# Performance work log

Measured on AMD Instinct MI355X. Metric: run time of the kernel, lower is better.

Reference implementation:

```python
import jax, jax.numpy as jnp
import numpy as np

B, S, D, KC = 32, 4096, 64, 256  # batch*heads, seq_len, head_dim, compressed dim


def setup_inputs() -> dict:
    key = jax.random.key(0)
    ks = jax.random.split(key, 7)
    return {
        "Q": jax.random.normal(ks[0], (B, S, D), dtype=jnp.float32),
        "K": jax.random.normal(ks[1], (B, S, D), dtype=jnp.float32),
        "V": jax.random.normal(ks[2], (B, S, D), dtype=jnp.float32),
        "E_w": jax.random.normal(ks[3], (KC, S), dtype=jnp.float32) * (1.0 / np.sqrt(S)),
        "E_b": jax.random.normal(ks[4], (KC,), dtype=jnp.float32) * 0.01,
        "F_w": jax.random.normal(ks[5], (KC, S), dtype=jnp.float32) * (1.0 / np.sqrt(S)),
        "F_b": jax.random.normal(ks[6], (KC,), dtype=jnp.float32) * 0.01,
    }


def reference(Q, K, V, E_w, E_b, F_w, F_b):
    # K: [B,S,D] -> transpose -> [B,D,S]; E proj over seq axis -> [B,D,KC]
    Ke = jnp.einsum("bsd,ks->bdk", K, E_w) + E_b  # [B, D, KC]
    # scores: Q @ E(K) -> [B, S, KC], scaled by sqrt(head_dim)
    scale = jnp.sqrt(jnp.asarray(D, dtype=Q.dtype))
    P = jnp.einsum("bsd,bdk->bsk", Q, Ke) / scale
    # causal mask: torch.triu(ones(S, KC)) keeps (i, j) where j >= i
    i = jnp.arange(S)[:, None]
    j = jnp.arange(KC)[None, :]
    keep = j >= i  # [S, KC]
    P = jnp.where(keep[None, :, :], P, jnp.asarray(-1e10, dtype=P.dtype))
    P = jax.nn.softmax(P, axis=-1)  # dropout p=0.0 -> identity
    # V: [B,S,D] -> [B,D,S]; F proj -> [B,D,KC]; transpose -> [B,KC,D]
    Vf = jnp.einsum("bsd,ks->bkd", V, F_w) + F_b[None, :, None]  # [B, KC, D]
    out = jnp.einsum("bsk,bkd->bsd", P, Vf)  # [B, S, D]
    return out
```

## Files before the change

kernel.cpp:

```cpp
#include <hip/hip_runtime.h>
#include <hip/hip_bf16.h>
#include <math.h>

#define NB  32
#define NS  4096
#define ND  64
#define NKC 256

#define BK    128
#define KHALF 2048
#define ASA   132
#define ASB   132

#define QSTR  72
#define PBSTR 264
#define VSTR  264

#define NKE ((size_t)NB * NKC * ND)

typedef __attribute__((ext_vector_type(8))) short short8;
typedef __attribute__((ext_vector_type(4))) float f32x4;

__device__ __forceinline__ short f2bf(float f) {
    union { float f; unsigned u; } v; v.f = f;
    return (short)((v.u + 0x7FFFu + ((v.u >> 16) & 1u)) >> 16);
}

template <typename AT>
__global__ __launch_bounds__(256, 2) void proj_sk(
    const AT* __restrict__ EwX, const AT* __restrict__ FwX,
    const float* __restrict__ K, const float* __restrict__ V,
    float* __restrict__ base)
{
    const int bid = blockIdx.x;
    const int r8 = bid & 7, mt = (bid >> 3) & 3, gq = bid >> 5;
    const int grp = gq * 8 + r8;
    const int kh = grp & 1, mm = (grp >> 1) & 1, b = grp >> 2;

    const AT* __restrict__ Ab    = mm ? FwX : EwX;
    const float* __restrict__ Bg = mm ? V   : K;
    float* __restrict__ Cout = base + (size_t)kh * 2 * NKE + (mm ? NKE : 0);

    const int t = threadIdx.x, wave = t >> 6, lane = t & 63;
    const int lm = lane & 15, g4 = lane >> 4;
    __shared__ short As[64 * ASA];
    __shared__ short Bs[64 * ASB];
    const size_t bBase = (size_t)b * NS * ND;
    const size_t aBase = (size_t)mt * 64 * NS;
    const int rA = t >> 4, jA = t & 15;
    const int dB = t & 31, sB = t >> 5;

    f32x4 acc[4];
#pragma unroll
    for (int nt = 0; nt < 4; ++nt) acc[nt] = (f32x4){0.f, 0.f, 0.f, 0.f};

    short8 pa[4];
    float4 paf[8];
    float2 pb[16];

    const int sBeg = kh * KHALF, sEnd = sBeg + KHALF;

#pragma unroll
    for (int i = 0; i < 4; ++i) {
        if constexpr (sizeof(AT) == 2) {
            pa[i] = *(const short8*)&Ab[aBase + (size_t)(i * 16 + rA) * NS + sBeg + jA * 8];
        } else {
            paf[2 * i]     = *(const float4*)&Ab[aBase + (size_t)(i * 16 + rA) * NS + sBeg + jA * 8];
            paf[2 * i + 1] = *(const float4*)&Ab[aBase + (size_t)(i * 16 + rA) * NS + sBeg + jA * 8 + 4];
        }
    }
#pragma unroll
    for (int h = 0; h < 2; ++h)
#pragma unroll
        for (int i = 0; i < 8; ++i)
            pb[h * 8 + i] = *(const float2*)&Bg[bBase + (size_t)(sBeg + h * 64 + sB * 8 + i) * ND + dB * 2];

    for (int s0 = sBeg; s0 < sEnd; s0 += BK) {
#pragma unroll
        for (int i = 0; i < 4; ++i) {
            if constexpr (sizeof(AT) == 2) {
                *(short8*)&As[(i * 16 + rA) * ASA + jA * 8] = pa[i];
            } else {
                short8 w;
                w[0] = f2bf(paf[2 * i].x);     w[1] = f2bf(paf[2 * i].y);
                w[2] = f2bf(paf[2 * i].z);     w[3] = f2bf(paf[2 * i].w);
                w[4] = f2bf(paf[2 * i + 1].x); w[5] = f2bf(paf[2 * i + 1].y);
                w[6] = f2bf(paf[2 * i + 1].z); w[7] = f2bf(paf[2 * i + 1].w);
                *(short8*)&As[(i * 16 + rA) * ASA + jA * 8] = w;
            }
        }
#pragma unroll
        for (int h = 0; h < 2; ++h) {
            short8 w0, w1;
#pragma unroll
            for (int i = 0; i < 8; ++i) {
                w0[i] = f2bf(pb[h * 8 + i].x);
                w1[i] = f2bf(pb[h * 8 + i].y);
            }
            *(short8*)&Bs[(dB * 2 + 0) * ASB + h * 64 + sB * 8] = w0;
            *(short8*)&Bs[(dB * 2 + 1) * ASB + h * 64 + sB * 8] = w1;
        }
        __syncthreads();

        if (s0 + BK < sEnd) {
            const int sn = s0 + BK;
#pragma unroll
            for (int i = 0; i < 4; ++i) {
                if constexpr (sizeof(AT) == 2) {
                    pa[i] = *(const short8*)&Ab[aBase + (size_t)(i * 16 + rA) * NS + sn + jA * 8];
                } else {
                    paf[2 * i]     = *(const float4*)&Ab[aBase + (size_t)(i * 16 + rA) * NS + sn + jA * 8];
                    paf[2 * i + 1] = *(const float4*)&Ab[aBase + (size_t)(i * 16 + rA) * NS + sn + jA * 8 + 4];
                }
            }
#pragma unroll
            for (int h = 0; h < 2; ++h)
#pragma unroll
                for (int i = 0; i < 8; ++i)
                    pb[h * 8 + i] = *(const float2*)&Bg[bBase + (size_t)(sn + h * 64 + sB * 8 + i) * ND + dB * 2];
        }

#pragma unroll
        for (int ks = 0; ks < BK; ks += 32) {
            short8 aF = *(const short8*)&As[(wave * 16 + lm) * ASA + ks + g4 * 8];
#pragma unroll
            for (int nt = 0; nt < 4; ++nt) {
                short8 bF = *(const short8*)&Bs[(nt * 16 + lm) * ASB + ks + g4 * 8];
                acc[nt] = __builtin_amdgcn_mfma_f32_16x16x32_bf16(aF, bF, acc[nt], 0, 0, 0);
            }
        }
        __syncthreads();
    }

#pragma unroll
    for (int nt = 0; nt < 4; ++nt)
#pragma unroll
        for (int rr = 0; rr < 4; ++rr) {
            int kc = mt * 64 + wave * 16 + g4 * 4 + rr;
            Cout[((size_t)b * NKC + kc) * ND + nt * 16 + lm] = acc[nt][rr];
        }
}

__global__ __launch_bounds__(256) void fuse(
    const float* __restrict__ base, const float* __restrict__ Eb,
    const float* __restrict__ Fb, short* __restrict__ KeB,
    short* __restrict__ VtB, float* __restrict__ ps)
{
    const int x = blockIdx.x, b = blockIdx.y, t = threadIdx.x;
    const int kb = x * 16;
    const float* Ka  = base;
    const float* Va  = base + NKE;
    const float* Kb_ = base + 2 * NKE;
    const float* Vb  = base + 3 * NKE;
    __shared__ float vt[16][65];
    const int kci = t >> 6, d = t & 63;

#pragma unroll
    for (int i = 0; i < 4; ++i) {
        int kc = kb + kci * 4 + i;
        size_t off = ((size_t)b * NKC + kc) * ND + d;
        KeB[off] = f2bf(Ka[off] + Kb_[off] + Eb[kc]);
        vt[kci * 4 + i][d] = Va[off] + Vb[off] + Fb[kc];
    }
    __syncthreads();
    if (t < 64) {
        float s = 0.f;
        short8 w0, w1;
#pragma unroll
        for (int i = 0; i < 8; ++i) { float v = vt[i][t];     s += v; w0[i] = f2bf(v); }
#pragma unroll
        for (int i = 0; i < 8; ++i) { float v = vt[8 + i][t]; s += v; w1[i] = f2bf(v); }
        ps[((size_t)b * 16 + x) * 64 + t] = s;
        short* dst = &VtB[((size_t)b * ND + t) * NKC + kb];
        *(short8*)&dst[0] = w0;
        *(short8*)&dst[8] = w1;
    }
}

__global__ __launch_bounds__(256) void attn_new(
    const float* __restrict__ Q,  const short* __restrict__ KeB,
    const short* __restrict__ VtB, const float* __restrict__ ps,
    float* __restrict__ out)
{
    const int x = blockIdx.x, b = blockIdx.y, t = threadIdx.x;

    if (x >= 8) {
        __shared__ float mvs[64];
        if (t < 64) {
            float s = 0.f;
#pragma unroll
            for (int i = 0; i < 16; ++i) s += ps[((size_t)b * 16 + i) * 64 + t];
            mvs[t] = s * (1.f / 256.f);
        }
        __syncthreads();
        const int r0 = 256 + (x - 8) * 64;
#pragma unroll
        for (int i = 0; i < 4; ++i) {
            int idx = i * 256 + t, row = idx >> 4, q = idx & 15;
            *(float4*)&out[((size_t)b * NS + r0 + row) * ND + q * 4] =
                *(const float4*)&mvs[q * 4];
        }
        return;
    }

    const int s0 = x * 32;
    const int wave = t >> 6, lane = t & 63, lm = lane & 15, g = lane >> 4;
    __shared__ short Qs[32 * QSTR];
    __shared__ short PsB[32 * PBSTR];
    __shared__ short VfT[64 * VSTR];
    __shared__ float rsums[32][4];

    {
        int row = t >> 3, dq = t & 7;
        size_t off = ((size_t)b * NS + s0 + row) * ND + dq * 8;
        float4 q0 = *(const float4*)&Q[off], q1 = *(const float4*)&Q[off + 4];
        short8 w;
        w[0] = f2bf(q0.x); w[1] = f2bf(q0.y); w[2] = f2bf(q0.z); w[3] = f2bf(q0.w);
        w[4] = f2bf(q1.x); w[5] = f2bf(q1.y); w[6] = f2bf(q1.z); w[7] = f2bf(q1.w);
        *(short8*)&Qs[row * QSTR + dq * 8] = w;
    }
    {
        const int d = t >> 2, q4 = t & 3;
        const short* src = &VtB[((size_t)b * ND + d) * NKC + q4 * 64];
#pragma unroll
        for (int i = 0; i < 8; ++i)
            *(short8*)&VfT[d * VSTR + q4 * 64 + i * 8] = *(const short8*)&src[i * 8];
    }
    __syncthreads();

    f32x4 accP[2][4];
#pragma unroll
    for (int rt = 0; rt < 2; ++rt)
#pragma unroll
        for (int kk = 0; kk < 4; ++kk) accP[rt][kk] = (f32x4){0.f, 0.f, 0.f, 0.f};
#pragma unroll
    for (int kk = 0; kk < 4; ++kk) {
        int kt = wave * 4 + kk;
#pragma unroll
        for (int ks2 = 0; ks2 < 2; ++ks2) {
            short8 bf = *(const short8*)&KeB[((size_t)b * NKC + kt * 16 + lm) * ND + ks2 * 32 + g * 8];
#pragma unroll
            for (int rt = 0; rt < 2; ++rt) {
                short8 aq = *(const short8*)&Qs[(rt * 16 + lm) * QSTR + ks2 * 32 + g * 8];
                accP[rt][kk] = __builtin_amdgcn_mfma_f32_16x16x32_bf16(aq, bf, accP[rt][kk], 0, 0, 0);
            }
        }
    }
#pragma unroll
    for (int rt = 0; rt < 2; ++rt)
#pragma unroll
        for (int r = 0; r < 4; ++r) {
            float s = 0.f;
            int rowg = s0 + rt * 16 + g * 4 + r;
#pragma unroll
            for (int kk = 0; kk < 4; ++kk) {
                int col = wave * 64 + kk * 16 + lm;
                float e = (col >= rowg) ? __expf(accP[rt][kk][r] * 0.125f) : 0.f;
                accP[rt][kk][r] = e;
                s += e;
            }
#pragma unroll
            for (int off = 1; off <= 8; off <<= 1) s += __shfl_xor(s, off, 64);
            if (lm == 0) rsums[rt * 16 + g * 4 + r][wave] = s;
        }
    __syncthreads();
#pragma unroll
    for (int rt = 0; rt < 2; ++rt)
#pragma unroll
        for (int r = 0; r < 4; ++r) {
            float4 rs = *(const float4*)&rsums[rt * 16 + g * 4 + r][0];
            float inv = 1.f / (rs.x + rs.y + rs.z + rs.w);
#pragma unroll
            for (int kk = 0; kk < 4; ++kk)
                PsB[(rt * 16 + g * 4 + r) * PBSTR + wave * 64 + kk * 16 + lm] =
                    f2bf(accP[rt][kk][r] * inv);
        }
    __syncthreads();

    f32x4 oa[2];
    oa[0] = (f32x4){0.f, 0.f, 0.f, 0.f};
    oa[1] = (f32x4){0.f, 0.f, 0.f, 0.f};
    for (int ks = x; ks < 8; ++ks) {
        short8 bv = *(const short8*)&VfT[(wave * 16 + lm) * VSTR + ks * 32 + g * 8];
#pragma unroll
        for (int rt = 0; rt < 2; ++rt) {
            short8 av = *(const short8*)&PsB[(rt * 16 + lm) * PBSTR + ks * 32 + g * 8];
            oa[rt] = __builtin_amdgcn_mfma_f32_16x16x32_bf16(av, bv, oa[rt], 0, 0, 0);
        }
    }
#pragma unroll
    for (int rt = 0; rt < 2; ++rt)
#pragma unroll
        for (int r = 0; r < 4; ++r)
            out[((size_t)b * NS + s0 + rt * 16 + g * 4 + r) * ND + wave * 16 + lm] = oa[rt][r];
}

__global__ __launch_bounds__(256) void attn_old(
    const float* __restrict__ Q,  const float* __restrict__ base,
    const float* __restrict__ Eb, const float* __restrict__ Fb,
    float* __restrict__ out)
{
    const int x = blockIdx.x, b = blockIdx.y, t = threadIdx.x;
    const float* KeTa = base;
    const float* Vfa  = base + NKE;
    const float* KeTb = base + 2 * NKE;
    const float* Vfb  = base + 3 * NKE;

    if (x >= 8) {
        __shared__ float pq[16][64];
        __shared__ float mvs[64];
        const int kg = t >> 4, dq = t & 15;
        float4 s4 = (float4){0.f, 0.f, 0.f, 0.f};
        for (int p = 0; p < 16; ++p) {
            int k = p * 16 + kg;
            float4 v = *(const float4*)&Vfa[((size_t)b * NKC + k) * ND + dq * 4];
            float4 u = *(const float4*)&Vfb[((size_t)b * NKC + k) * ND + dq * 4];
            float fb = Fb[k];
            s4.x += (v.x + u.x) + fb; s4.y += (v.y + u.y) + fb;
            s4.z += (v.z + u.z) + fb; s4.w += (v.w + u.w) + fb;
        }
        *(float4*)&pq[kg][dq * 4] = s4;
        __syncthreads();
        if (t < 64) {
            float m = 0.f;
#pragma unroll
            for (int i = 0; i < 16; ++i) m += pq[i][t];
            mvs[t] = m * (1.f / 256.f);
        }
        __syncthreads();
        const int r0 = 256 + (x - 8) * 64;
#pragma unroll
        for (int i = 0; i < 4; ++i) {
            int idx = i * 256 + t, row = idx >> 4, q = idx & 15;
            *(float4*)&out[((size_t)b * NS + r0 + row) * ND + q * 4] =
                *(const float4*)&mvs[q * 4];
        }
        return;
    }

    const int s0 = x * 32;
    const int wave = t >> 6, lane = t & 63, lm = lane & 15, g = lane >> 4;
    __shared__ short Qs[32 * QSTR];
    __shared__ short PsB[32 * PBSTR];
    __shared__ short VfT[64 * VSTR];
    __shared__ float rsums[32][4];

    {
        int row = t >> 3, dq = t & 7;
        size_t off = ((size_t)b * NS + s0 + row) * ND + dq * 8;
        float4 q0 = *(const float4*)&Q[off], q1 = *(const float4*)&Q[off + 4];
        short8 w;
        w[0] = f2bf(q0.x); w[1] = f2bf(q0.y); w[2] = f2bf(q0.z); w[3] = f2bf(q0.w);
        w[4] = f2bf(q1.x); w[5] = f2bf(q1.y); w[6] = f2bf(q1.z); w[7] = f2bf(q1.w);
        *(short8*)&Qs[row * QSTR + dq * 8] = w;
    }
    {
        const int dB = t & 31, sB = t >> 5;
#pragma unroll
        for (int pass = 0; pass < 4; ++pass) {
            int kb = pass * 64 + sB * 8;
            float2 v[8]; float fb[8];
#pragma unroll
            for (int i = 0; i < 8; ++i) {
                float2 a = *(const float2*)&Vfa[((size_t)b * NKC + kb + i) * ND + dB * 2];
                float2 c = *(const float2*)&Vfb[((size_t)b * NKC + kb + i) * ND + dB * 2];
                v[i]  = (float2){a.x + c.x, a.y + c.y};
                fb[i] = Fb[kb + i];
            }
            short8 w0, w1;
#pragma unroll
            for (int i = 0; i < 8; ++i) {
                w0[i] = f2bf(v[i].x + fb[i]);
                w1[i] = f2bf(v[i].y + fb[i]);
            }
            *(short8*)&VfT[(dB * 2 + 0) * VSTR + kb] = w0;
            *(short8*)&VfT[(dB * 2 + 1) * VSTR + kb] = w1;
        }
    }
    __syncthreads();

    f32x4 accP[2][4];
#pragma unroll
    for (int rt = 0; rt < 2; ++rt)
#pragma unroll
        for (int kk = 0; kk < 4; ++kk) accP[rt][kk] = (f32x4){0.f, 0.f, 0.f, 0.f};
#pragma unroll
    for (int kk = 0; kk < 4; ++kk) {
        int kt = wave * 4 + kk;
        float ebv = Eb[kt * 16 + lm];
#pragma unroll
        for (int ks2 = 0; ks2 < 2; ++ks2) {
            const size_t koff = ((size_t)b * NKC + kt * 16 + lm) * ND + ks2 * 32 + g * 8;
            float4 c0 = *(const float4*)&KeTa[koff], c1 = *(const float4*)&KeTa[koff + 4];
            float4 e0 = *(const float4*)&KeTb[koff], e1 = *(const float4*)&KeTb[koff + 4];
            short8 bf;
            bf[0] = f2bf((c0.x + e0.x) + ebv); bf[1] = f2bf((c0.y + e0.y) + ebv);
            bf[2] = f2bf((c0.z + e0.z) + ebv); bf[3] = f2bf((c0.w + e0.w) + ebv);
            bf[4] = f2bf((c1.x + e1.x) + ebv); bf[5] = f2bf((c1.y + e1.y) + ebv);
            bf[6] = f2bf((c1.z + e1.z) + ebv); bf[7] = f2bf((c1.w + e1.w) + ebv);
#pragma unroll
            for (int rt = 0; rt < 2; ++rt) {
                short8 aq = *(const short8*)&Qs[(rt * 16 + lm) * QSTR + ks2 * 32 + g * 8];
                accP[rt][kk] = __builtin_amdgcn_mfma_f32_16x16x32_bf16(aq, bf, accP[rt][kk], 0, 0, 0);
            }
        }
    }
#pragma unroll
    for (int rt = 0; rt < 2; ++rt)
#pragma unroll
        for (int r = 0; r < 4; ++r) {
            float s = 0.f;
            int rowg = s0 + rt * 16 + g * 4 + r;
#pragma unroll
            for (int kk = 0; kk < 4; ++kk) {
                int col = wave * 64 + kk * 16 + lm;
                float e = (col >= rowg) ? __expf(accP[rt][kk][r] * 0.125f) : 0.f;
                accP[rt][kk][r] = e;
                s += e;
            }
#pragma unroll
            for (int off = 1; off <= 8; off <<= 1) s += __shfl_xor(s, off, 64);
            if (lm == 0) rsums[rt * 16 + g * 4 + r][wave] = s;
        }
    __syncthreads();
#pragma unroll
    for (int rt = 0; rt < 2; ++rt)
#pragma unroll
        for (int r = 0; r < 4; ++r) {
            float4 rs = *(const float4*)&rsums[rt * 16 + g * 4 + r][0];
            float inv = 1.f / (rs.x + rs.y + rs.z + rs.w);
#pragma unroll
            for (int kk = 0; kk < 4; ++kk)
                PsB[(rt * 16 + g * 4 + r) * PBSTR + wave * 64 + kk * 16 + lm] =
                    f2bf(accP[rt][kk][r] * inv);
        }
    __syncthreads();

    f32x4 oa[2];
    oa[0] = (f32x4){0.f, 0.f, 0.f, 0.f};
    oa[1] = (f32x4){0.f, 0.f, 0.f, 0.f};
    for (int ks = x; ks < 8; ++ks) {
        short8 bv = *(const short8*)&VfT[(wave * 16 + lm) * VSTR + ks * 32 + g * 8];
#pragma unroll
        for (int rt = 0; rt < 2; ++rt) {
            short8 av = *(const short8*)&PsB[(rt * 16 + lm) * PBSTR + ks * 32 + g * 8];
            oa[rt] = __builtin_amdgcn_mfma_f32_16x16x32_bf16(av, bv, oa[rt], 0, 0, 0);
        }
    }
#pragma unroll
    for (int rt = 0; rt < 2; ++rt)
#pragma unroll
        for (int r = 0; r < 4; ++r)
            out[((size_t)b * NS + s0 + rt * 16 + g * 4 + r) * ND + wave * 16 + lm] = oa[rt][r];
}

extern "C" void kernel_launch(void* const* d_in, const int* in_sizes, int n_in,
                              void* d_out, int out_size, void* d_ws, size_t ws_size,
                              hipStream_t stream) {
    (void)in_sizes; (void)n_in; (void)out_size;
    const float* Q  = (const float*)d_in[0];
    const float* K  = (const float*)d_in[1];
    const float* V  = (const float*)d_in[2];
    const float* Ew = (const float*)d_in[3];
    const float* Eb = (const float*)d_in[4];
    const float* Fw = (const float*)d_in[5];
    const float* Fb = (const float*)d_in[6];
    float* out = (float*)d_out;

    float* base = (float*)d_ws;
    const size_t MB = 1024u * 1024u;

    proj_sk<float><<<dim3(512), 256, 0, stream>>>(Ew, Fw, K, V, base);

    if (ws_size >= 11 * MB) {
        short* KeB = (short*)(base + 4 * NKE);
        short* VtB = KeB + NKE;
        float* ps  = (float*)(VtB + NKE);
        fuse<<<dim3(16, NB), 256, 0, stream>>>(base, Eb, Fb, KeB, VtB, ps);
        attn_new<<<dim3(68, NB), 256, 0, stream>>>(Q, KeB, VtB, ps, out);
    } else {
        attn_old<<<dim3(68, NB), 256, 0, stream>>>(Q, base, Eb, Fb, out);
    }
}
```

Measured before the change: 183.7 us.

## Pre-convert projection weights to bf16 and widen K/V loads to float4

Adds a prep kernel that converts E_w and F_w to bf16 once per call, so the projection kernel's 128 blocks per weight tile re-read half the bytes and skip repeated conversion. It also changes the K/V staging loads from float2 to float4 per thread, with a new thread mapping into shared memory. The cost is an extra kernel launch, an extra pass over both weight matrices, and a larger workspace requirement; the new path runs only when the workspace is at least 15 MB, otherwise the old path is used.

```diff
diff --git a/kernel.cpp b/kernel.cpp
--- a/kernel.cpp
+++ b/kernel.cpp
@@ -24,6 +24,23 @@
 __device__ __forceinline__ short f2bf(float f) {
     union { float f; unsigned u; } v; v.f = f;
     return (short)((v.u + 0x7FFFu + ((v.u >> 16) & 1u)) >> 16);
+}
+
+__global__ __launch_bounds__(256) void prep(
+    const float* __restrict__ Ew, const float* __restrict__ Fw,
+    short* __restrict__ EwB, short* __restrict__ FwB)
+{
+    const int gid = blockIdx.x * 256 + threadIdx.x;
+    const int half = (NKC * NS) / 8;
+    const float* src = (gid < half) ? Ew : Fw;
+    short* dst       = (gid < half) ? EwB : FwB;
+    const int i8 = (gid < half) ? gid : gid - half;
+    float4 a = *(const float4*)&src[(size_t)i8 * 8];
+    float4 c = *(const float4*)&src[(size_t)i8 * 8 + 4];
+    short8 w;
+    w[0] = f2bf(a.x); w[1] = f2bf(a.y); w[2] = f2bf(a.z); w[3] = f2bf(a.w);
+    w[4] = f2bf(c.x); w[5] = f2bf(c.y); w[6] = f2bf(c.z); w[7] = f2bf(c.w);
+    *(short8*)&dst[(size_t)i8 * 8] = w;
 }
 
 template <typename AT>
@@ -48,7 +65,7 @@
     const size_t bBase = (size_t)b * NS * ND;
     const size_t aBase = (size_t)mt * 64 * NS;
     const int rA = t >> 4, jA = t & 15;
-    const int dB = t & 31, sB = t >> 5;
+    const int dQ = t & 15, sG = t >> 4;
 
     f32x4 acc[4];
 #pragma unroll
@@ -56,7 +73,7 @@
 
     short8 pa[4];
     float4 paf[8];
-    float2 pb[16];
+    float4 pbv[8];
 
     const int sBeg = kh * KHALF, sEnd = sBeg + KHALF;
 
@@ -70,10 +87,8 @@
         }
     }
 #pragma unroll
-    for (int h = 0; h < 2; ++h)
-#pragma unroll
-        for (int i = 0; i < 8; ++i)
-            pb[h * 8 + i] = *(const float2*)&Bg[bBase + (size_t)(sBeg + h * 64 + sB * 8 + i) * ND + dB * 2];
+    for (int i = 0; i < 8; ++i)
+        pbv[i] = *(const float4*)&Bg[bBase + (size_t)(sBeg + sG * 8 + i) * ND + dQ * 4];
 
     for (int s0 = sBeg; s0 < sEnd; s0 += BK) {
 #pragma unroll
@@ -89,16 +104,17 @@
                 *(short8*)&As[(i * 16 + rA) * ASA + jA * 8] = w;
             }
         }
-#pragma unroll
-        for (int h = 0; h < 2; ++h) {
-            short8 w0, w1;
+        {
+            short8 w0, w1, w2, w3;
 #pragma unroll
             for (int i = 0; i < 8; ++i) {
-                w0[i] = f2bf(pb[h * 8 + i].x);
-                w1[i] = f2bf(pb[h * 8 + i].y);
-            }
-            *(short8*)&Bs[(dB * 2 + 0) * ASB + h * 64 + sB * 8] = w0;
-            *(short8*)&Bs[(dB * 2 + 1) * ASB + h * 64 + sB * 8] = w1;
+                w0[i] = f2bf(pbv[i].x); w1[i] = f2bf(pbv[i].y);
+                w2[i] = f2bf(pbv[i].z); w3[i] = f2bf(pbv[i].w);
+            }
+            *(short8*)&Bs[(dQ * 4 + 0) * ASB + sG * 8] = w0;
+            *(short8*)&Bs[(dQ * 4 + 1) * ASB + sG * 8] = w1;
+            *(short8*)&Bs[(dQ * 4 + 2) * ASB + sG * 8] = w2;
+            *(short8*)&Bs[(dQ * 4 + 3) * ASB + sG * 8] = w3;
         }
         __syncthreads();
 
@@ -114,10 +130,8 @@
                 }
             }
 #pragma unroll
-            for (int h = 0; h < 2; ++h)
-#pragma unroll
-                for (int i = 0; i < 8; ++i)
-                    pb[h * 8 + i] = *(const float2*)&Bg[bBase + (size_t)(sn + h * 64 + sB * 8 + i) * ND + dB * 2];
+            for (int i = 0; i < 8; ++i)
+                pbv[i] = *(const float4*)&Bg[bBase + (size_t)(sn + sG * 8 + i) * ND + dQ * 4];
         }
 
 #pragma unroll
@@ -470,15 +484,18 @@
     float* base = (float*)d_ws;
     const size_t MB = 1024u * 1024u;
 
-    proj_sk<float><<<dim3(512), 256, 0, stream>>>(Ew, Fw, K, V, base);
-
-    if (ws_size >= 11 * MB) {
-        short* KeB = (short*)(base + 4 * NKE);
+    if (ws_size >= 15 * MB) {
+        short* EwB = (short*)(base + 4 * NKE);
+        short* FwB = EwB + (size_t)NKC * NS;
+        short* KeB = FwB + (size_t)NKC * NS;
         short* VtB = KeB + NKE;
         float* ps  = (float*)(VtB + NKE);
+        prep<<<dim3(1024), 256, 0, stream>>>(Ew, Fw, EwB, FwB);
+        proj_sk<short><<<dim3(512), 256, 0, stream>>>(EwB, FwB, K, V, base);
         fuse<<<dim3(16, NB), 256, 0, stream>>>(base, Eb, Fb, KeB, VtB, ps);
         attn_new<<<dim3(68, NB), 256, 0, stream>>>(Q, KeB, VtB, ps, out);
     } else {
+        proj_sk<float><<<dim3(512), 256, 0, stream>>>(Ew, Fw, K, V, base);
         attn_old<<<dim3(68, NB), 256, 0, stream>>>(Q, base, Eb, Fb, out);
     }
 }
```

Result: faster. 170.7 us (-7.0%).
